# Kernel tuning notes

Measured on AMD Instinct MI355X. Metric: run time of the kernel, lower is better.

## Reference

```python
import jax, jax.numpy as jnp
import numpy as np

S = 30.0
M = 0.5
EPS = 1e-07


def setup_inputs() -> dict:
    key = jax.random.key(0)
    k1, k2, k3 = jax.random.split(key, 3)
    B, D, C = 1024, 512, 100000
    embeddings = jax.random.normal(k1, (B, D), dtype=jnp.float32)
    # xavier_uniform for weight [C, D]
    limit = float(np.sqrt(6.0 / (C + D)))
    weight = jax.random.uniform(k2, (C, D), dtype=jnp.float32, minval=-limit, maxval=limit)
    labels = jax.random.randint(k3, (B,), 0, C, dtype=jnp.int64)
    return {"embeddings": embeddings, "weight": weight, "labels": labels}


def _l2norm(x, axis=-1):
    # matches F.normalize(p=2, eps=1e-12)
    n = jnp.linalg.norm(x, axis=axis, keepdims=True)
    return x / jnp.maximum(n, 1e-12)


def reference(embeddings, weight, labels):
    # cosine: [B, C] = normalized embeddings @ normalized weight^T
    cosine = _l2norm(embeddings) @ _l2norm(weight).T
    B = cosine.shape[0]
    rows = jnp.arange(B)
    # margin transform only on the target logit per row (same math as
    # one_hot combine: cos(acos(clamp(c)) + m) at the label column)
    tgt = cosine[rows, labels]
    theta = jnp.arccos(jnp.clip(tgt, -1.0 + EPS, 1.0 - EPS))
    target_logit = jnp.cos(theta + M)
    output = cosine.at[rows, labels].set(target_logit)
    return output * S
```

## Files before the change

kernel.cpp:

```cpp
#include <hip/hip_runtime.h>
#include <hip/hip_bf16.h>

typedef __attribute__((ext_vector_type(8))) short bf16x8;
typedef __attribute__((ext_vector_type(4))) float f32x4;

#define B_ROWS 1024
#define C_COLS 100000
#define K_DIM  512
#define BM 128
#define BN 128
#define BK 32
#define SCALE_S 30.0f
#define MARGIN_M 0.5f
#define EPS_C 1e-7f

__device__ __forceinline__ void gload_lds16(const __hip_bfloat16* g, __hip_bfloat16* l) {
    __builtin_amdgcn_global_load_lds((const __attribute__((address_space(1))) void*)g,
                                     (__attribute__((address_space(3))) void*)l,
                                     16, 0, 0);
}

__global__ __launch_bounds__(256) void l2norm_bf16_rows(const float* __restrict__ in,
                                                        __hip_bfloat16* __restrict__ out,
                                                        int nrows) {
    int wid  = (int)((blockIdx.x * blockDim.x + threadIdx.x) >> 6);
    int lane = threadIdx.x & 63;
    if (wid >= nrows) return;
    const float4* rp = (const float4*)(in + (size_t)wid * K_DIM);
    float4 v0 = rp[lane * 2];
    float4 v1 = rp[lane * 2 + 1];
    float ss = v0.x * v0.x + v0.y * v0.y + v0.z * v0.z + v0.w * v0.w
             + v1.x * v1.x + v1.y * v1.y + v1.z * v1.z + v1.w * v1.w;
#pragma unroll
    for (int off = 32; off > 0; off >>= 1) ss += __shfl_xor(ss, off, 64);
    float scale = 1.0f / fmaxf(sqrtf(ss), 1e-12f);
    union { __hip_bfloat16 h[8]; int4 q; } u;
    u.h[0] = __float2bfloat16(v0.x * scale);
    u.h[1] = __float2bfloat16(v0.y * scale);
    u.h[2] = __float2bfloat16(v0.z * scale);
    u.h[3] = __float2bfloat16(v0.w * scale);
    u.h[4] = __float2bfloat16(v1.x * scale);
    u.h[5] = __float2bfloat16(v1.y * scale);
    u.h[6] = __float2bfloat16(v1.z * scale);
    u.h[7] = __float2bfloat16(v1.w * scale);
    ((int4*)(out + (size_t)wid * K_DIM))[lane] = u.q;
}

__global__ __launch_bounds__(256, 2) void arcface_gemm(
        const __hip_bfloat16* __restrict__ A,
        const __hip_bfloat16* __restrict__ W,
        float* __restrict__ out) {
    __shared__ __hip_bfloat16 sA[2][BM * BK];
    __shared__ __hip_bfloat16 sB[2][BN * BK];

    const int bid = blockIdx.x;
    const int per = gridDim.x >> 3;
    const int nid = (bid & 7) * per + (bid >> 3);
    const int mt = nid & 7;
    const int nt = nid >> 3;
    const long m0 = (long)mt * BM;
    const long n0 = (long)nt * BN;

    const int tid  = threadIdx.x;
    const int lane = tid & 63;
    const int w    = tid >> 6;
    const int wr = w >> 1, wc = w & 1;
    const int lidx = lane & 15, lk = lane >> 4;

    const int srow   = lane >> 2;
    const int schunk = (lane & 3) ^ (srow & 3);

    f32x4 acc[4][4];
#pragma unroll
    for (int m = 0; m < 4; ++m)
#pragma unroll
        for (int n = 0; n < 4; ++n) acc[m][n] = (f32x4){0.f, 0.f, 0.f, 0.f};

#define STAGE(buf, kt) do {                                                        \
        _Pragma("unroll")                                                          \
        for (int i = 0; i < 2; ++i) {                                              \
            int rloc = (w * 2 + i) * 16 + srow;                                    \
            long gar = m0 + rloc;                                                  \
            gload_lds16(A + gar * K_DIM + (long)(kt) * BK + schunk * 8,            \
                        &sA[buf][(w * 2 + i) * 512]);                              \
            long gbr = n0 + rloc;                                                  \
            if (gbr >= C_COLS) gbr = C_COLS - 1;                                   \
            gload_lds16(W + gbr * K_DIM + (long)(kt) * BK + schunk * 8,            \
                        &sB[buf][(w * 2 + i) * 512]);                              \
        }                                                                          \
    } while (0)

    STAGE(0, 0);
    __syncthreads();
    int cur = 0;
    const int NKT = K_DIM / BK;
    for (int kt = 0; kt < NKT; ++kt) {
        if (kt + 1 < NKT) STAGE(cur ^ 1, kt + 1);
        bf16x8 af[4], bfv[4];
        const int ck = (lk ^ (lidx & 3)) * 8;
#pragma unroll
        for (int m = 0; m < 4; ++m)
            af[m] = *(const bf16x8*)&sA[cur][(wr * 64 + m * 16 + lidx) * BK + ck];
#pragma unroll
        for (int n = 0; n < 4; ++n)
            bfv[n] = *(const bf16x8*)&sB[cur][(wc * 64 + n * 16 + lidx) * BK + ck];
#pragma unroll
        for (int m = 0; m < 4; ++m)
#pragma unroll
            for (int n = 0; n < 4; ++n)
                acc[m][n] = __builtin_amdgcn_mfma_f32_16x16x32_bf16(af[m], bfv[n],
                                                                    acc[m][n], 0, 0, 0);
        __syncthreads();
        cur ^= 1;
    }
#undef STAGE

    const long colbase = n0 + wc * 64 + lidx;
#pragma unroll
    for (int m = 0; m < 4; ++m) {
        long rowb = m0 + wr * 64 + m * 16 + lk * 4;
#pragma unroll
        for (int n = 0; n < 4; ++n) {
            long gcol = colbase + n * 16;
            if (gcol < C_COLS) {
#pragma unroll
                for (int j = 0; j < 4; ++j)
                    out[(rowb + j) * (long)C_COLS + gcol] = acc[m][n][j] * SCALE_S;
            }
        }
    }
}

__global__ void margin_fixup(float* __restrict__ out, const int* __restrict__ labels,
                             int nrows) {
    int b = blockIdx.x * blockDim.x + threadIdx.x;
    if (b >= nrows) return;
    int lab = labels[b];
    size_t idx = (size_t)b * C_COLS + (size_t)lab;
    float c = out[idx] * (1.0f / SCALE_S);
    c = fminf(fmaxf(c, -1.0f + EPS_C), 1.0f - EPS_C);
    float t = acosf(c) + MARGIN_M;
    out[idx] = cosf(t) * SCALE_S;
}

extern "C" void kernel_launch(void* const* d_in, const int* in_sizes, int n_in,
                              void* d_out, int out_size, void* d_ws, size_t ws_size,
                              hipStream_t stream) {
    const float* emb = (const float*)d_in[0];
    const float* wgt = (const float*)d_in[1];
    const int* labels = (const int*)d_in[2];
    float* out = (float*)d_out;

    __hip_bfloat16* embb = (__hip_bfloat16*)d_ws;
    __hip_bfloat16* wgtb = (__hip_bfloat16*)((char*)d_ws + (size_t)B_ROWS * K_DIM * 2);

    l2norm_bf16_rows<<<B_ROWS / 4, 256, 0, stream>>>(emb, embb, B_ROWS);
    l2norm_bf16_rows<<<C_COLS / 4, 256, 0, stream>>>(wgt, wgtb, C_COLS);
    const int ntiles = (C_COLS + BN - 1) / BN;
    arcface_gemm<<<8 * ntiles, 256, 0, stream>>>(embb, wgtb, out);
    margin_fixup<<<(B_ROWS + 255) / 256, 256, 0, stream>>>(out, labels, B_ROWS);
}
```

Before: 712.8 us.

## Enlarge GEMM tiles to 256x256x64 with 8 waves and interleaved staging pipeline

```diff
diff --git a/kernel.cpp b/kernel.cpp
--- a/kernel.cpp
+++ b/kernel.cpp
@@ -7,17 +7,25 @@
 #define B_ROWS 1024
 #define C_COLS 100000
 #define K_DIM  512
-#define BM 128
-#define BN 128
-#define BK 32
 #define SCALE_S 30.0f
 #define MARGIN_M 0.5f
 #define EPS_C 1e-7f
+
+#define BM 256
+#define BN 256
+#define BK 64
+#define NKT (K_DIM / BK)
 
 __device__ __forceinline__ void gload_lds16(const __hip_bfloat16* g, __hip_bfloat16* l) {
     __builtin_amdgcn_global_load_lds((const __attribute__((address_space(1))) void*)g,
                                      (__attribute__((address_space(3))) void*)l,
                                      16, 0, 0);
+}
+
+__device__ __forceinline__ void barrier_fenced() {
+    asm volatile("" ::: "memory");
+    __builtin_amdgcn_s_barrier();
+    asm volatile("" ::: "memory");
 }
 
 __global__ __launch_bounds__(256) void l2norm_bf16_rows(const float* __restrict__ in,
@@ -27,108 +35,181 @@
     int lane = threadIdx.x & 63;
     if (wid >= nrows) return;
     const float4* rp = (const float4*)(in + (size_t)wid * K_DIM);
-    float4 v0 = rp[lane * 2];
-    float4 v1 = rp[lane * 2 + 1];
+    float4 v0 = rp[lane];
+    float4 v1 = rp[lane + 64];
     float ss = v0.x * v0.x + v0.y * v0.y + v0.z * v0.z + v0.w * v0.w
              + v1.x * v1.x + v1.y * v1.y + v1.z * v1.z + v1.w * v1.w;
 #pragma unroll
     for (int off = 32; off > 0; off >>= 1) ss += __shfl_xor(ss, off, 64);
     float scale = 1.0f / fmaxf(sqrtf(ss), 1e-12f);
-    union { __hip_bfloat16 h[8]; int4 q; } u;
-    u.h[0] = __float2bfloat16(v0.x * scale);
-    u.h[1] = __float2bfloat16(v0.y * scale);
-    u.h[2] = __float2bfloat16(v0.z * scale);
-    u.h[3] = __float2bfloat16(v0.w * scale);
-    u.h[4] = __float2bfloat16(v1.x * scale);
-    u.h[5] = __float2bfloat16(v1.y * scale);
-    u.h[6] = __float2bfloat16(v1.z * scale);
-    u.h[7] = __float2bfloat16(v1.w * scale);
-    ((int4*)(out + (size_t)wid * K_DIM))[lane] = u.q;
-}
-
-__global__ __launch_bounds__(256, 2) void arcface_gemm(
+    union { __hip_bfloat16 h[4]; int2 q; } a, b;
+    a.h[0] = __float2bfloat16(v0.x * scale);
+    a.h[1] = __float2bfloat16(v0.y * scale);
+    a.h[2] = __float2bfloat16(v0.z * scale);
+    a.h[3] = __float2bfloat16(v0.w * scale);
+    b.h[0] = __float2bfloat16(v1.x * scale);
+    b.h[1] = __float2bfloat16(v1.y * scale);
+    b.h[2] = __float2bfloat16(v1.z * scale);
+    b.h[3] = __float2bfloat16(v1.w * scale);
+    int2* op = (int2*)(out + (size_t)wid * K_DIM);
+    op[lane]      = a.q;
+    op[lane + 64] = b.q;
+}
+
+__global__ __launch_bounds__(512, 2) void arcface_gemm(
         const __hip_bfloat16* __restrict__ A,
         const __hip_bfloat16* __restrict__ W,
         float* __restrict__ out) {
-    __shared__ __hip_bfloat16 sA[2][BM * BK];
-    __shared__ __hip_bfloat16 sB[2][BN * BK];
-
-    const int bid = blockIdx.x;
-    const int per = gridDim.x >> 3;
-    const int nid = (bid & 7) * per + (bid >> 3);
-    const int mt = nid & 7;
-    const int nt = nid >> 3;
+    __shared__ __hip_bfloat16 sA[2 * 2 * 256 * 32];
+    __shared__ __hip_bfloat16 sB[2 * 2 * 256 * 32];
+
+    const int nwg = (int)gridDim.x;
+    const int q8 = nwg >> 3, r8 = nwg & 7;
+    const int xcd = (int)blockIdx.x & 7, ii = (int)blockIdx.x >> 3;
+    const int wg = (xcd < r8 ? xcd * (q8 + 1) : r8 * (q8 + 1) + (xcd - r8) * q8) + ii;
+    const int mt = wg & 3, nt = wg >> 2;
     const long m0 = (long)mt * BM;
     const long n0 = (long)nt * BN;
 
-    const int tid  = threadIdx.x;
+    const int tid  = (int)threadIdx.x;
     const int lane = tid & 63;
     const int w    = tid >> 6;
-    const int wr = w >> 1, wc = w & 1;
+    const int wm   = w >> 2;
+    const int wn   = w & 3;
     const int lidx = lane & 15, lk = lane >> 4;
 
-    const int srow   = lane >> 2;
-    const int schunk = (lane & 3) ^ (srow & 3);
-
-    f32x4 acc[4][4];
-#pragma unroll
-    for (int m = 0; m < 4; ++m)
+    const int srow  = tid >> 2;
+    const int sslot = (tid & 3) ^ (srow & 3);
+
+#define STAGE_A(buf, kh, kt) do {                                                   \
+        gload_lds16(A + (m0 + srow) * K_DIM + (kt) * BK + (kh) * 32 + sslot * 8,    \
+                    &sA[((((buf) * 2 + (kh)) * 256) * 32) + (0 * 512 + tid) * 8]);  \
+        gload_lds16(A + (m0 + 128 + srow) * K_DIM + (kt) * BK + (kh) * 32 + sslot * 8, \
+                    &sA[((((buf) * 2 + (kh)) * 256) * 32) + (1 * 512 + tid) * 8]);  \
+    } while (0)
+
+#define STAGE_B(buf, kh, kt) do {                                                   \
+        long r0 = n0 + srow;       if (r0 >= C_COLS) r0 = C_COLS - 1;               \
+        long r1 = n0 + 128 + srow; if (r1 >= C_COLS) r1 = C_COLS - 1;               \
+        gload_lds16(W + r0 * K_DIM + (kt) * BK + (kh) * 32 + sslot * 8,             \
+                    &sB[((((buf) * 2 + (kh)) * 256) * 32) + (0 * 512 + tid) * 8]);  \
+        gload_lds16(W + r1 * K_DIM + (kt) * BK + (kh) * 32 + sslot * 8,             \
+                    &sB[((((buf) * 2 + (kh)) * 256) * 32) + (1 * 512 + tid) * 8]);  \
+    } while (0)
+
+#define LDA(dst, c, kh, mh) do {                                                    \
+        _Pragma("unroll")                                                           \
+        for (int i = 0; i < 4; ++i) {                                               \
+            int row = wm * 128 + (mh) * 64 + i * 16 + lidx;                         \
+            dst[i] = *(const bf16x8*)&sA[(((c) * 2 + (kh)) * 256 + row) * 32        \
+                                         + ((lk ^ (lidx & 3)) * 8)];                \
+        }                                                                           \
+    } while (0)
+
+#define LDB(dst, c, kh) do {                                                        \
+        _Pragma("unroll")                                                           \
+        for (int n = 0; n < 4; ++n) {                                               \
+            int row = wn * 64 + n * 16 + lidx;                                      \
+            dst[n] = *(const bf16x8*)&sB[(((c) * 2 + (kh)) * 256 + row) * 32        \
+                                         + ((lk ^ (lidx & 3)) * 8)];                \
+        }                                                                           \
+    } while (0)
+
+#define MFMA16(mh, av_, bv_) do {                                                   \
+        __builtin_amdgcn_s_setprio(1);                                              \
+        _Pragma("unroll")                                                           \
+        for (int m = 0; m < 4; ++m)                                                 \
+            _Pragma("unroll")                                                       \
+            for (int n = 0; n < 4; ++n)                                             \
+                acc[(mh) * 4 + m][n] = __builtin_amdgcn_mfma_f32_16x16x32_bf16(     \
+                    av_[m], bv_[n], acc[(mh) * 4 + m][n], 0, 0, 0);                 \
+        __builtin_amdgcn_s_setprio(0);                                              \
+    } while (0)
+
+#define WAIT_LGKM0() do { asm volatile("s_waitcnt lgkmcnt(0)" ::: "memory"); \
+                          __builtin_amdgcn_sched_barrier(0); } while (0)
+#define WAIT_VM4()   asm volatile("s_waitcnt vmcnt(4)" ::: "memory")
+#define WAIT_VM0()   asm volatile("s_waitcnt vmcnt(0)" ::: "memory")
+
+    f32x4 acc[8][4];
+#pragma unroll
+    for (int m = 0; m < 8; ++m)
 #pragma unroll
         for (int n = 0; n < 4; ++n) acc[m][n] = (f32x4){0.f, 0.f, 0.f, 0.f};
 
-#define STAGE(buf, kt) do {                                                        \
-        _Pragma("unroll")                                                          \
-        for (int i = 0; i < 2; ++i) {                                              \
-            int rloc = (w * 2 + i) * 16 + srow;                                    \
-            long gar = m0 + rloc;                                                  \
-            gload_lds16(A + gar * K_DIM + (long)(kt) * BK + schunk * 8,            \
-                        &sA[buf][(w * 2 + i) * 512]);                              \
-            long gbr = n0 + rloc;                                                  \
-            if (gbr >= C_COLS) gbr = C_COLS - 1;                                   \
-            gload_lds16(W + gbr * K_DIM + (long)(kt) * BK + schunk * 8,            \
-                        &sB[buf][(w * 2 + i) * 512]);                              \
-        }                                                                          \
-    } while (0)
-
-    STAGE(0, 0);
-    __syncthreads();
-    int cur = 0;
-    const int NKT = K_DIM / BK;
-    for (int kt = 0; kt < NKT; ++kt) {
-        if (kt + 1 < NKT) STAGE(cur ^ 1, kt + 1);
-        bf16x8 af[4], bfv[4];
-        const int ck = (lk ^ (lidx & 3)) * 8;
-#pragma unroll
-        for (int m = 0; m < 4; ++m)
-            af[m] = *(const bf16x8*)&sA[cur][(wr * 64 + m * 16 + lidx) * BK + ck];
-#pragma unroll
-        for (int n = 0; n < 4; ++n)
-            bfv[n] = *(const bf16x8*)&sB[cur][(wc * 64 + n * 16 + lidx) * BK + ck];
-#pragma unroll
-        for (int m = 0; m < 4; ++m)
-#pragma unroll
-            for (int n = 0; n < 4; ++n)
-                acc[m][n] = __builtin_amdgcn_mfma_f32_16x16x32_bf16(af[m], bfv[n],
-                                                                    acc[m][n], 0, 0, 0);
-        __syncthreads();
-        cur ^= 1;
+    STAGE_A(0, 0, 0); STAGE_B(0, 0, 0);
+    STAGE_A(0, 1, 0); STAGE_B(0, 1, 0);
+    WAIT_VM4();
+    barrier_fenced();
+
+    bf16x8 av[4], bv[4];
+    for (int t = 0; t < NKT - 1; ++t) {
+        const int c = t & 1, nb = c ^ 1;
+        LDA(av, c, 0, 0); LDB(bv, c, 0);
+        STAGE_A(nb, 0, t + 1);
+        barrier_fenced(); WAIT_LGKM0();
+        MFMA16(0, av, bv);
+        barrier_fenced();
+        LDA(av, c, 0, 1);
+        STAGE_B(nb, 0, t + 1);
+        barrier_fenced(); WAIT_LGKM0();
+        MFMA16(1, av, bv);
+        WAIT_VM4();
+        barrier_fenced();
+        LDA(av, c, 1, 0); LDB(bv, c, 1);
+        STAGE_A(nb, 1, t + 1);
+        barrier_fenced(); WAIT_LGKM0();
+        MFMA16(0, av, bv);
+        barrier_fenced();
+        LDA(av, c, 1, 1);
+        STAGE_B(nb, 1, t + 1);
+        barrier_fenced(); WAIT_LGKM0();
+        MFMA16(1, av, bv);
+        WAIT_VM4();
+        barrier_fenced();
     }
-#undef STAGE
-
-    const long colbase = n0 + wc * 64 + lidx;
-#pragma unroll
-    for (int m = 0; m < 4; ++m) {
-        long rowb = m0 + wr * 64 + m * 16 + lk * 4;
-#pragma unroll
-        for (int n = 0; n < 4; ++n) {
-            long gcol = colbase + n * 16;
-            if (gcol < C_COLS) {
+    {
+        const int c = (NKT - 1) & 1;
+        LDA(av, c, 0, 0); LDB(bv, c, 0);
+        barrier_fenced(); WAIT_LGKM0();
+        MFMA16(0, av, bv);
+        barrier_fenced();
+        LDA(av, c, 0, 1);
+        barrier_fenced(); WAIT_LGKM0();
+        MFMA16(1, av, bv);
+        WAIT_VM0();
+        barrier_fenced();
+        LDA(av, c, 1, 0); LDB(bv, c, 1);
+        barrier_fenced(); WAIT_LGKM0();
+        MFMA16(0, av, bv);
+        barrier_fenced();
+        LDA(av, c, 1, 1);
+        barrier_fenced(); WAIT_LGKM0();
+        MFMA16(1, av, bv);
+    }
+
+    const long colb = n0 + wn * 64 + lidx;
+#pragma unroll
+    for (int mf = 0; mf < 8; ++mf) {
+        long rowb = m0 + wm * 128 + mf * 16 + lk * 4;
+#pragma unroll
+        for (int nf = 0; nf < 4; ++nf) {
+            long gc = colb + nf * 16;
+            if (gc < C_COLS) {
 #pragma unroll
                 for (int j = 0; j < 4; ++j)
-                    out[(rowb + j) * (long)C_COLS + gcol] = acc[m][n][j] * SCALE_S;
+                    out[(rowb + j) * (long)C_COLS + gc] = acc[mf][nf][j] * SCALE_S;
             }
         }
     }
+#undef STAGE_A
+#undef STAGE_B
+#undef LDA
+#undef LDB
+#undef MFMA16
+#undef WAIT_LGKM0
+#undef WAIT_VM4
+#undef WAIT_VM0
 }
 
 __global__ void margin_fixup(float* __restrict__ out, const int* __restrict__ labels,
@@ -156,7 +237,9 @@
 
     l2norm_bf16_rows<<<B_ROWS / 4, 256, 0, stream>>>(emb, embb, B_ROWS);
     l2norm_bf16_rows<<<C_COLS / 4, 256, 0, stream>>>(wgt, wgtb, C_COLS);
+
     const int ntiles = (C_COLS + BN - 1) / BN;
-    arcface_gemm<<<8 * ntiles, 256, 0, stream>>>(embb, wgtb, out);
+    arcface_gemm<<<4 * ntiles, 512, 0, stream>>>(embb, wgtb, out);
+
     margin_fixup<<<(B_ROWS + 255) / 256, 256, 0, stream>>>(out, labels, B_ROWS);
 }
```

New measurement: 703.6 us (median of 2 runs). Within noise of the previous version (-1.3%).
